# Kernel optimization log

Measured on AMD Instinct MI355X. Metric: run time of the kernel, lower is better.

## Reference

```python
import jax, jax.numpy as jnp
import numpy as np

N, D = 8192, 128
TEMPERATURE = 128.0


def setup_inputs() -> dict:
    key = jax.random.key(0)
    kx, ka = jax.random.split(key)
    x = jax.random.normal(kx, (N, D), dtype=jnp.float32)
    a = jax.random.normal(ka, (N, D), dtype=jnp.float32)
    return {"x": x, "a": a}


def reference(x, a):
    """uLSIF loss, 2D branch, exp_parameterization='inner_product', reduction='mean'.

    L_i = -2 * sim[i,i] + mean_{j != i} sim[i,j]^2,  sim = exp(x @ a.T / T)
    """
    n = x.shape[0]
    sim = jnp.exp(jnp.matmul(x, a.T) / TEMPERATURE)  # [N, N]
    sim_pos = jnp.diagonal(sim)                      # [N]
    # off-diagonal squared mean without a boolean-mask gather:
    # sum_j sim[i,j]^2 - sim[i,i]^2, divided by (N-1)
    row_sq_sum = jnp.sum(sim * sim, axis=1)          # [N]
    sim_neg_square = (row_sq_sum - sim_pos * sim_pos) / (n - 1)
    lora_loss = -2.0 * sim_pos + sim_neg_square      # [N]
    return jnp.mean(lora_loss)
```

## Files before the change

### kernel.cpp

```cpp
#include <hip/hip_runtime.h>


#define NN 8192
#define DD 128

typedef __attribute__((ext_vector_type(4))) float f32x4;
typedef __attribute__((ext_vector_type(8))) _Float16 f16x8;

__global__ void conv_diag_kernel(const float4* __restrict__ x, const float4* __restrict__ a,
                                 char* __restrict__ xf, char* __restrict__ af,
                                 double* __restrict__ s1p, double* __restrict__ s3p) {
    const float C2 = (float)(2.0 / (128.0 * 0.69314718055994530942));
    int t = threadIdx.x;
    int i = blockIdx.x * 256 + t;
    int row = i >> 5;
    int q   = i & 31;
    int ks  = q >> 3;
    int l   = (((q & 7) >> 1) << 4) | (row & 15);
    int f   = (row >> 4) * 4 + ks;
    size_t off = (size_t)f * 1024 + (size_t)l * 16 + (size_t)(i & 1) * 8;

    float4 xv = x[i];
    float4 av = a[i];
    ushort4 xu, au;
    xu.x = __builtin_bit_cast(unsigned short, (_Float16)xv.x);
    xu.y = __builtin_bit_cast(unsigned short, (_Float16)xv.y);
    xu.z = __builtin_bit_cast(unsigned short, (_Float16)xv.z);
    xu.w = __builtin_bit_cast(unsigned short, (_Float16)xv.w);
    au.x = __builtin_bit_cast(unsigned short, (_Float16)(av.x * C2));
    au.y = __builtin_bit_cast(unsigned short, (_Float16)(av.y * C2));
    au.z = __builtin_bit_cast(unsigned short, (_Float16)(av.z * C2));
    au.w = __builtin_bit_cast(unsigned short, (_Float16)(av.w * C2));
    *(ushort4*)(xf + off) = xu;
    *(ushort4*)(af + off) = au;

    float d = xv.x * av.x + xv.y * av.y + xv.z * av.z + xv.w * av.w;
#pragma unroll
    for (int o = 16; o > 0; o >>= 1) d += __shfl_down(d, o, 32);

    __shared__ double rr[8];
    if ((t & 31) == 0) rr[t >> 5] = exp((double)d * (1.0 / 128.0));
    __syncthreads();
    if (t == 0) {
        double s1 = 0.0, s3 = 0.0;
#pragma unroll
        for (int k = 0; k < 8; ++k) { s1 += rr[k]; s3 += rr[k] * rr[k]; }
        s1p[blockIdx.x] = s1;
        s3p[blockIdx.x] = s3;
    }
}

__global__ __launch_bounds__(512, 2) void gemm_exp_sum(const f16x8* __restrict__ xf,
                                                       const f16x8* __restrict__ af,
                                                       double* __restrict__ s2p) {
    const int tid  = threadIdx.x;
    const int lane = tid & 63;
    const int wid  = tid >> 6;
    const int bm    = blockIdx.x >> 3;
    const int chunk = blockIdx.x & 7;
    const int wm = wid >> 1;
    const int wn = wid & 1;

    const int fA0 = (bm * 16 + wm * 4) * 4;
    f16x8 afr[4][4];
#pragma unroll
    for (int mi = 0; mi < 4; ++mi)
#pragma unroll
        for (int ks = 0; ks < 4; ++ks)
            afr[mi][ks] = xf[(size_t)(fA0 + mi * 4 + ks) * 64 + lane];

    const int fB0 = (chunk * 64 + wn * 2) * 4;

    f16x8 b0[2][4], b1[2][4];
#pragma unroll
    for (int ni = 0; ni < 2; ++ni)
#pragma unroll
        for (int ks = 0; ks < 4; ++ks)
            b0[ni][ks] = af[(size_t)(fB0 + ni * 4 + ks) * 64 + lane];

    f32x4 acc[4][2];
    float ls0 = 0.f, ls1 = 0.f, ls2 = 0.f, ls3 = 0.f;

#define PREFETCH(B, S)                                                              \
    {                                                                               \
        const int sc = (S) > 15 ? 15 : (S);                                         \
        _Pragma("unroll") for (int ni = 0; ni < 2; ++ni)                            \
            _Pragma("unroll") for (int ks = 0; ks < 4; ++ks)                        \
                B[ni][ks] = af[(size_t)(fB0 + sc * 16 + ni * 4 + ks) * 64 + lane];  \
    }

#define COMPUTE(B)                                                                  \
    {                                                                               \
        _Pragma("unroll") for (int mi = 0; mi < 4; ++mi)                            \
            _Pragma("unroll") for (int ni = 0; ni < 2; ++ni)                        \
                acc[mi][ni] = f32x4{0.f, 0.f, 0.f, 0.f};                            \
        _Pragma("unroll") for (int ks = 0; ks < 4; ++ks)                            \
            _Pragma("unroll") for (int mi = 0; mi < 4; ++mi)                        \
                _Pragma("unroll") for (int ni = 0; ni < 2; ++ni)                    \
                    acc[mi][ni] = __builtin_amdgcn_mfma_f32_16x16x32_f16(           \
                        afr[mi][ks], B[ni][ks], acc[mi][ni], 0, 0, 0);              \
        _Pragma("unroll") for (int mi = 0; mi < 4; ++mi)                            \
            _Pragma("unroll") for (int ni = 0; ni < 2; ++ni) {                      \
                ls0 += __builtin_amdgcn_exp2f(acc[mi][ni][0]);                      \
                ls1 += __builtin_amdgcn_exp2f(acc[mi][ni][1]);                      \
                ls2 += __builtin_amdgcn_exp2f(acc[mi][ni][2]);                      \
                ls3 += __builtin_amdgcn_exp2f(acc[mi][ni][3]);                      \
            }                                                                       \
    }

#pragma unroll 1
    for (int s = 0; s < 16; s += 2) {
        PREFETCH(b1, s + 1);
        COMPUTE(b0);
        PREFETCH(b0, s + 2);
        COMPUTE(b1);
    }
#undef PREFETCH
#undef COMPUTE

    float lsum = (ls0 + ls1) + (ls2 + ls3);
#pragma unroll
    for (int o = 32; o > 0; o >>= 1) lsum += __shfl_down(lsum, o);

    __shared__ double wred[8];
    if (lane == 0) wred[wid] = (double)lsum;
    __syncthreads();
    if (tid == 0) {
        double s = 0.0;
#pragma unroll
        for (int k = 0; k < 8; ++k) s += wred[k];
        s2p[blockIdx.x] = s;
    }
}

__global__ void finalize_kernel(const double* __restrict__ s1p, const double* __restrict__ s3p,
                                const double* __restrict__ s2p, float* __restrict__ out) {
    int t = threadIdx.x;
    double v1 = s1p[t];
    double v3 = s3p[t];
    double v2 = (t < 256) ? s2p[t] : 0.0;
#pragma unroll
    for (int o = 32; o > 0; o >>= 1) {
        v1 += __shfl_down(v1, o);
        v3 += __shfl_down(v3, o);
        v2 += __shfl_down(v2, o);
    }
    __shared__ double r1[16], r2[16], r3[16];
    int wid = t >> 6, lane = t & 63;
    if (lane == 0) { r1[wid] = v1; r2[wid] = v2; r3[wid] = v3; }
    __syncthreads();
    if (t == 0) {
        double S1 = 0.0, S2 = 0.0, S3 = 0.0;
#pragma unroll
        for (int k = 0; k < 16; ++k) { S1 += r1[k]; S2 += r2[k]; S3 += r3[k]; }
        double res = (-2.0 * S1 + (S2 - S3) / (double)(NN - 1)) / (double)NN;
        out[0] = (float)res;
    }
}

extern "C" void kernel_launch(void* const* d_in, const int* in_sizes, int n_in,
                              void* d_out, int out_size, void* d_ws, size_t ws_size,
                              hipStream_t stream) {
    const float* x = (const float*)d_in[0];
    const float* a = (const float*)d_in[1];
    float* out = (float*)d_out;
    char* ws = (char*)d_ws;

    double* s1p = (double*)ws;
    double* s3p = (double*)(ws + 8192);
    double* s2p = (double*)(ws + 16384);
    char*   xf  = ws + 32768;
    char*   af  = ws + 32768 + (size_t)NN * DD * 2;

    conv_diag_kernel<<<1024, 256, 0, stream>>>((const float4*)x, (const float4*)a,
                                               xf, af, s1p, s3p);
    gemm_exp_sum<<<256, 512, 0, stream>>>((const f16x8*)xf, (const f16x8*)af, s2p);
    finalize_kernel<<<1, 1024, 0, stream>>>(s1p, s3p, s2p, out);
}
```

Measured before the change: 102.2 us.

## Repartition GEMM-exp into smaller blocks with swizzled panel/chunk mapping

The fused GEMM+exp kernel now launches 1024 blocks of 256 threads instead of 256 blocks of 512. Each warp holds a 32-row A fragment (down from 64) and streams the full B chunk per block, using a fully unrolled loop in place of the explicit double-buffered prefetch. Block indices are swizzled so that consecutive blocks share B chunks across panels. The aim is better occupancy and load balance across CUs, at the cost of lower arithmetic intensity per loaded B fragment and reliance on the compiler to schedule the loads.

```diff
diff --git a/kernel.cpp b/kernel.cpp
--- a/kernel.cpp
+++ b/kernel.cpp
@@ -50,87 +50,71 @@
     }
 }
 
-__global__ __launch_bounds__(512, 2) void gemm_exp_sum(const f16x8* __restrict__ xf,
+__global__ __launch_bounds__(256, 4) void gemm_exp_sum(const f16x8* __restrict__ xf,
                                                        const f16x8* __restrict__ af,
                                                        double* __restrict__ s2p) {
     const int tid  = threadIdx.x;
     const int lane = tid & 63;
-    const int wid  = tid >> 6;
-    const int bm    = blockIdx.x >> 3;
-    const int chunk = blockIdx.x & 7;
-    const int wm = wid >> 1;
-    const int wn = wid & 1;
+    const int wm   = tid >> 6;
+    const int wg    = (blockIdx.x & 7) * 128 + (blockIdx.x >> 3);
+    const int panel = wg >> 4;
+    const int chunk = wg & 15;
 
-    const int fA0 = (bm * 16 + wm * 4) * 4;
-    f16x8 afr[4][4];
+    const int fA0 = (panel * 8 + wm * 2) * 4;
+    f16x8 afr[2][4];
 #pragma unroll
-    for (int mi = 0; mi < 4; ++mi)
+    for (int mi = 0; mi < 2; ++mi)
 #pragma unroll
         for (int ks = 0; ks < 4; ++ks)
             afr[mi][ks] = xf[(size_t)(fA0 + mi * 4 + ks) * 64 + lane];
 
-    const int fB0 = (chunk * 64 + wn * 2) * 4;
+    const int fB0 = chunk * 128;
+    float ls0 = 0.f, ls1 = 0.f, ls2 = 0.f, ls3 = 0.f;
 
-    f16x8 b0[2][4], b1[2][4];
 #pragma unroll
-    for (int ni = 0; ni < 2; ++ni)
+    for (int s = 0; s < 16; ++s) {
+        f16x8 b[2][4];
+#pragma unroll
+        for (int ni = 0; ni < 2; ++ni)
+#pragma unroll
+            for (int ks = 0; ks < 4; ++ks)
+                b[ni][ks] = af[(size_t)(fB0 + (s * 2 + ni) * 4 + ks) * 64 + lane];
+
+        f32x4 acc[2][2];
+#pragma unroll
+        for (int mi = 0; mi < 2; ++mi)
+#pragma unroll
+            for (int ni = 0; ni < 2; ++ni) acc[mi][ni] = f32x4{0.f, 0.f, 0.f, 0.f};
+
 #pragma unroll
         for (int ks = 0; ks < 4; ++ks)
-            b0[ni][ks] = af[(size_t)(fB0 + ni * 4 + ks) * 64 + lane];
+#pragma unroll
+            for (int mi = 0; mi < 2; ++mi)
+#pragma unroll
+                for (int ni = 0; ni < 2; ++ni)
+                    acc[mi][ni] = __builtin_amdgcn_mfma_f32_16x16x32_f16(
+                        afr[mi][ks], b[ni][ks], acc[mi][ni], 0, 0, 0);
 
-    f32x4 acc[4][2];
-    float ls0 = 0.f, ls1 = 0.f, ls2 = 0.f, ls3 = 0.f;
-
-#define PREFETCH(B, S)                                                              \
-    {                                                                               \
-        const int sc = (S) > 15 ? 15 : (S);                                         \
-        _Pragma("unroll") for (int ni = 0; ni < 2; ++ni)                            \
-            _Pragma("unroll") for (int ks = 0; ks < 4; ++ks)                        \
-                B[ni][ks] = af[(size_t)(fB0 + sc * 16 + ni * 4 + ks) * 64 + lane];  \
+#pragma unroll
+        for (int mi = 0; mi < 2; ++mi)
+#pragma unroll
+            for (int ni = 0; ni < 2; ++ni) {
+                ls0 += __builtin_amdgcn_exp2f(acc[mi][ni][0]);
+                ls1 += __builtin_amdgcn_exp2f(acc[mi][ni][1]);
+                ls2 += __builtin_amdgcn_exp2f(acc[mi][ni][2]);
+                ls3 += __builtin_amdgcn_exp2f(acc[mi][ni][3]);
+            }
     }
-
-#define COMPUTE(B)                                                                  \
-    {                                                                               \
-        _Pragma("unroll") for (int mi = 0; mi < 4; ++mi)                            \
-            _Pragma("unroll") for (int ni = 0; ni < 2; ++ni)                        \
-                acc[mi][ni] = f32x4{0.f, 0.f, 0.f, 0.f};                            \
-        _Pragma("unroll") for (int ks = 0; ks < 4; ++ks)                            \
-            _Pragma("unroll") for (int mi = 0; mi < 4; ++mi)                        \
-                _Pragma("unroll") for (int ni = 0; ni < 2; ++ni)                    \
-                    acc[mi][ni] = __builtin_amdgcn_mfma_f32_16x16x32_f16(           \
-                        afr[mi][ks], B[ni][ks], acc[mi][ni], 0, 0, 0);              \
-        _Pragma("unroll") for (int mi = 0; mi < 4; ++mi)                            \
-            _Pragma("unroll") for (int ni = 0; ni < 2; ++ni) {                      \
-                ls0 += __builtin_amdgcn_exp2f(acc[mi][ni][0]);                      \
-                ls1 += __builtin_amdgcn_exp2f(acc[mi][ni][1]);                      \
-                ls2 += __builtin_amdgcn_exp2f(acc[mi][ni][2]);                      \
-                ls3 += __builtin_amdgcn_exp2f(acc[mi][ni][3]);                      \
-            }                                                                       \
-    }
-
-#pragma unroll 1
-    for (int s = 0; s < 16; s += 2) {
-        PREFETCH(b1, s + 1);
-        COMPUTE(b0);
-        PREFETCH(b0, s + 2);
-        COMPUTE(b1);
-    }
-#undef PREFETCH
-#undef COMPUTE
 
     float lsum = (ls0 + ls1) + (ls2 + ls3);
 #pragma unroll
     for (int o = 32; o > 0; o >>= 1) lsum += __shfl_down(lsum, o);
 
-    __shared__ double wred[8];
-    if (lane == 0) wred[wid] = (double)lsum;
+    __shared__ double wred[4];
+    if (lane == 0) wred[wm] = (double)lsum;
     __syncthreads();
-    if (tid == 0) {
-        double s = 0.0;
-#pragma unroll
-        for (int k = 0; k < 8; ++k) s += wred[k];
-        s2p[blockIdx.x] = s;
-    }
+    if (tid == 0)
+        s2p[blockIdx.x] = (wred[0] + wred[1]) + (wred[2] + wred[3]);
 }
 
 __global__ void finalize_kernel(const double* __restrict__ s1p, const double* __restrict__ s3p,
@@ -138,7 +122,7 @@
     int t = threadIdx.x;
     double v1 = s1p[t];
     double v3 = s3p[t];
-    double v2 = (t < 256) ? s2p[t] : 0.0;
+    double v2 = s2p[t];
 #pragma unroll
     for (int o = 32; o > 0; o >>= 1) {
         v1 += __shfl_down(v1, o);
@@ -174,6 +158,6 @@
 
     conv_diag_kernel<<<1024, 256, 0, stream>>>((const float4*)x, (const float4*)a,
                                                xf, af, s1p, s3p);
-    gemm_exp_sum<<<256, 512, 0, stream>>>((const f16x8*)xf, (const f16x8*)af, s2p);
+    gemm_exp_sum<<<1024, 256, 0, stream>>>((const f16x8*)xf, (const f16x8*)af, s2p);
     finalize_kernel<<<1, 1024, 0, stream>>>(s1p, s3p, s2p, out);
 }
```

Result: faster. 83.63 us (-18.1%).
